# Optimization experiments

Hardware: AMD Instinct MI355X
Metric: run time of the kernel (lower is better)

## Reference

```python
import jax, jax.numpy as jnp
import numpy as np

B, H, E, K = 8192, 1024, 8, 2


def setup_inputs() -> dict:
    key = jax.random.key(0)
    k1, k2, k3 = jax.random.split(key, 3)
    x = jax.random.normal(k1, (B, H), dtype=jnp.float32)
    gate_w = jax.random.normal(k2, (H, E), dtype=jnp.float32) / np.sqrt(H)
    expert_w = jax.random.normal(k3, (E, H, H), dtype=jnp.float32) / np.sqrt(H)
    return {"x": x, "gate_w": gate_w, "expert_w": expert_w}


def reference(x, gate_w, expert_w):
    # Gate: logits over experts, top-k routing, softmax over the k selected logits
    logits = x @ gate_w                               # [B, E]
    top_w, top_idx = jax.lax.top_k(logits, K)         # [B, K]
    top_w = jax.nn.softmax(top_w, axis=-1)            # softmax over the K selected
    # Combine weights scattered back to [B, E]; zero for unselected experts
    combine = jnp.zeros((x.shape[0], expert_w.shape[0]), dtype=x.dtype)
    combine = combine.at[jnp.arange(x.shape[0])[:, None], top_idx].add(top_w)
    # Expert GEMMs (dense dispatch reference: every expert on every token,
    # masked/weighted by combine; mathematically identical to gather/scatter)
    expert_out = jnp.einsum('bh,eho->beo', x, expert_w)   # [B, E, H]
    out = jnp.einsum('be,beo->bo', combine, expert_out)   # [B, H]
    return out
```

## Files before the change

### kernel.cpp

```cpp
#include <hip/hip_runtime.h>
#include <hip/hip_bf16.h>
#include <stdint.h>

#define B_TOK 8192
#define H_DIM 1024
#define E_NUM 8
#define NSLOT (2 * B_TOK)

typedef __attribute__((ext_vector_type(8))) short short8;
typedef __attribute__((ext_vector_type(4))) float floatx4;

__device__ __forceinline__ unsigned short f32_to_bf16_rne(float f) {
  union { float f; uint32_t u; } v; v.f = f;
  uint32_t u = v.u;
  uint32_t r = u + 0x7FFFu + ((u >> 16) & 1u);
  return (unsigned short)(r >> 16);
}
__device__ __forceinline__ float bf16_to_f32(unsigned short s) {
  union { uint32_t u; float f; } v; v.u = ((uint32_t)s) << 16;
  return v.f;
}

__global__ __launch_bounds__(256) void prep_kernel(const float* __restrict__ x,
                                                   const float* __restrict__ gw,
                                                   const float* __restrict__ ew,
                                                   unsigned short* __restrict__ xb,
                                                   unsigned short* __restrict__ wt,
                                                   int2* __restrict__ re,
                                                   float2* __restrict__ rw) {
  __shared__ float smem[E_NUM * 1028];
  int bid = blockIdx.x;
  int tid = threadIdx.x;
  if (bid < 2048) {
    float (*tile)[65] = (float(*)[65])smem;
    int e = bid >> 8;
    int n0 = ((bid >> 4) & 15) * 64, k0 = (bid & 15) * 64;
    const float* wb = ew + ((size_t)e * H_DIM + k0) * H_DIM + n0;
    unsigned short* wtb = wt + ((size_t)e * H_DIM + n0) * H_DIM + k0;
    int rr = tid >> 4, c4 = tid & 15;
#pragma unroll
    for (int j = 0; j < 4; ++j) {
      int r = rr + j * 16;
      float4 v = *(const float4*)(wb + (size_t)r * H_DIM + c4 * 4);
      tile[c4 * 4 + 0][r] = v.x;
      tile[c4 * 4 + 1][r] = v.y;
      tile[c4 * 4 + 2][r] = v.z;
      tile[c4 * 4 + 3][r] = v.w;
    }
    __syncthreads();
#pragma unroll
    for (int j = 0; j < 4; ++j) {
      int nr = rr + j * 16;
      float4 v = *(const float4*)&tile[nr][c4 * 4];
      ushort4 o;
      o.x = f32_to_bf16_rne(v.x); o.y = f32_to_bf16_rne(v.y);
      o.z = f32_to_bf16_rne(v.z); o.w = f32_to_bf16_rne(v.w);
      *(ushort4*)(wtb + (size_t)nr * H_DIM + c4 * 4) = o;
    }
  } else {
    int rb = bid - 2048;
    float (*gws)[1028] = (float(*)[1028])smem;
#pragma unroll
    for (int it = 0; it < 8; ++it) {
      int i4 = it * 256 + tid;
      float4 v = ((const float4*)gw)[i4];
      int h = i4 >> 1, e0 = (i4 & 1) * 4;
      gws[e0 + 0][h] = v.x;
      gws[e0 + 1][h] = v.y;
      gws[e0 + 2][h] = v.z;
      gws[e0 + 3][h] = v.w;
    }
    __syncthreads();
    int wid = tid >> 6, lane = tid & 63;
    for (int t = 0; t < 4; ++t) {
      int b = rb * 16 + wid * 4 + t;
      const float4* xr = (const float4*)(x + (size_t)b * H_DIM);
      ushort4* xbr = (ushort4*)(xb + (size_t)b * H_DIM);
      float acc[E_NUM];
#pragma unroll
      for (int e = 0; e < E_NUM; e++) acc[e] = 0.f;
#pragma unroll
      for (int it = 0; it < 4; ++it) {
        int c4 = it * 64 + lane;
        float4 v = xr[c4];
        ushort4 o;
        o.x = f32_to_bf16_rne(v.x); o.y = f32_to_bf16_rne(v.y);
        o.z = f32_to_bf16_rne(v.z); o.w = f32_to_bf16_rne(v.w);
        xbr[c4] = o;
        int h = c4 * 4;
#pragma unroll
        for (int e = 0; e < E_NUM; e++) {
          float4 g = *(const float4*)&gws[e][h];
          acc[e] += v.x * g.x + v.y * g.y + v.z * g.z + v.w * g.w;
        }
      }
#pragma unroll
      for (int e = 0; e < E_NUM; e++) {
#pragma unroll
        for (int off = 32; off; off >>= 1) acc[e] += __shfl_xor(acc[e], off, 64);
      }
      if (lane == 0) {
        int e0 = 0; float v0 = acc[0];
#pragma unroll
        for (int e = 1; e < E_NUM; e++) if (acc[e] > v0) { v0 = acc[e]; e0 = e; }
        int e1 = -1; float v1 = -1e30f;
#pragma unroll
        for (int e = 0; e < E_NUM; e++) if (e != e0 && acc[e] > v1) { v1 = acc[e]; e1 = e; }
        float s = expf(v1 - v0);
        float w0 = 1.0f / (1.0f + s);
        re[b] = make_int2(e0, e1);
        rw[b] = make_float2(w0, s * w0);
      }
    }
  }
}

__global__ __launch_bounds__(1024) void compact_kernel(const int2* __restrict__ re,
                                                       int* __restrict__ slot_tok,
                                                       int* __restrict__ yslot,
                                                       int* __restrict__ ebase,
                                                       int* __restrict__ ecnt) {
  __shared__ int wcnt[8][16];
  __shared__ int bless[16];
  int e = blockIdx.x;
  int tid = threadIdx.x, wid = tid >> 6, lane = tid & 63;
  int cless = 0;
  int flag[8];
  unsigned long long mm[8];
#pragma unroll
  for (int it = 0; it < 8; ++it) {
    int2 ee = re[it * 1024 + tid];
    cless += (ee.x < e) + (ee.y < e);
    bool f0 = (ee.x == e), f1 = (ee.y == e);
    flag[it] = f0 ? 1 : (f1 ? 2 : 0);
    mm[it] = __ballot(f0 || f1);
    if (lane == 0) wcnt[it][wid] = __popcll(mm[it]);
  }
#pragma unroll
  for (int off = 32; off; off >>= 1) cless += __shfl_xor(cless, off, 64);
  if (lane == 0) bless[wid] = cless;
  __syncthreads();
  int base = 0;
#pragma unroll
  for (int i = 0; i < 16; ++i) base += bless[i];
  int run = 0;
#pragma unroll
  for (int it = 0; it < 8; ++it) {
    int wbase = 0, total = 0;
#pragma unroll
    for (int i = 0; i < 16; ++i) { int v = wcnt[it][i]; if (i < wid) wbase += v; total += v; }
    if (flag[it]) {
      int pre = __popcll(mm[it] & ((1ull << lane) - 1ull));
      int s = base + run + wbase + pre;
      int t = it * 1024 + tid;
      slot_tok[s] = t;
      yslot[2 * t + (flag[it] == 1 ? 0 : 1)] = s;
    }
    run += total;
  }
  if (tid == 0) { ebase[e] = base; ecnt[e] = run; }
}

__device__ __forceinline__ void async_ld16(const void* g, void* l) {
  __builtin_amdgcn_global_load_lds((const __attribute__((address_space(1))) void*)g,
                                   (__attribute__((address_space(3))) void*)l, 16, 0, 0);
}

__global__ __launch_bounds__(256, 3) void moe_gemm_kernel(
    const unsigned short* __restrict__ xb,
    const unsigned short* __restrict__ wt,
    const int* __restrict__ ebase,
    const int* __restrict__ ecnt,
    const int* __restrict__ slot_tok,
    unsigned short* __restrict__ y) {
  int e = blockIdx.z;
  int c = ecnt[e];
  int m_idx = ((blockIdx.y >> 3) << 3) + blockIdx.x;
  int n_idx = blockIdx.y & 7;
  int m0 = m_idx * 128;
  if (m0 >= c) return;
  int base = ebase[e];
  int n0 = n_idx * 128;

  __shared__ __align__(16) unsigned short As[128 * 64];
  __shared__ __align__(16) unsigned short Bs[128 * 64];

  int tid = threadIdx.x, wid = tid >> 6, lane = tid & 63;
  int rloc = lane >> 3;
  int cl = lane & 7;
  const int* st = slot_tok + base;

  const unsigned short* gA[4];
  const unsigned short* gB[4];
  unsigned short* lA[4];
  unsigned short* lB[4];
#pragma unroll
  for (int j = 0; j < 4; ++j) {
    int rl = wid * 32 + j * 8 + rloc;
    int g = (cl ^ (rl & 7)) * 8;
    int ra = min(m0 + rl, c - 1);
    gA[j] = xb + (size_t)st[ra] * H_DIM + g;
    gB[j] = wt + ((size_t)e * H_DIM + n0 + rl) * H_DIM + g;
    lA[j] = As + (wid * 32 + j * 8) * 64;
    lB[j] = Bs + (wid * 32 + j * 8) * 64;
  }

  floatx4 acc[4][4];
#pragma unroll
  for (int a = 0; a < 4; ++a)
#pragma unroll
    for (int b = 0; b < 4; ++b)
#pragma unroll
      for (int q = 0; q < 4; ++q) acc[a][b][q] = 0.0f;

  int wm = (wid >> 1) * 64, wn = (wid & 1) * 64;
  int mr = lane & 15, kg = lane >> 4;
  int sw = mr & 7;

  for (int ks = 0; ks < 16; ++ks) {
    __syncthreads();
#pragma unroll
    for (int j = 0; j < 4; ++j) {
      async_ld16(gA[j], lA[j]);
      async_ld16(gB[j], lB[j]);
    }
#pragma unroll
    for (int j = 0; j < 4; ++j) { gA[j] += 64; gB[j] += 64; }
    __syncthreads();
#pragma unroll
    for (int kk = 0; kk < 2; ++kk) {
      int cb = ((kk * 4 + kg) ^ sw) * 8;
      short8 af[4], bfr[4];
#pragma unroll
      for (int t = 0; t < 4; ++t) {
        af[t]  = *(const short8*)(const void*)(As + (wm + t * 16 + mr) * 64 + cb);
        bfr[t] = *(const short8*)(const void*)(Bs + (wn + t * 16 + mr) * 64 + cb);
      }
#pragma unroll
      for (int tm = 0; tm < 4; ++tm)
#pragma unroll
        for (int tn = 0; tn < 4; ++tn)
          acc[tm][tn] = __builtin_amdgcn_mfma_f32_16x16x32_bf16(af[tm], bfr[tn], acc[tm][tn], 0, 0, 0);
    }
  }

#pragma unroll
  for (int tm = 0; tm < 4; ++tm) {
#pragma unroll
    for (int q = 0; q < 4; ++q) {
      int r = m0 + wm + tm * 16 + kg * 4 + q;
      if (r < c) {
        unsigned short* yrow = y + (size_t)(base + r) * H_DIM + n0 + wn + mr;
#pragma unroll
        for (int tn = 0; tn < 4; ++tn) yrow[tn * 16] = f32_to_bf16_rne(acc[tm][tn][q]);
      }
    }
  }
}

__global__ __launch_bounds__(256) void combine_kernel(const unsigned short* __restrict__ y,
                                                      const int* __restrict__ yslot,
                                                      const float2* __restrict__ rw,
                                                      float* __restrict__ out) {
  int wid = threadIdx.x >> 6, lane = threadIdx.x & 63;
  int t = blockIdx.x * 4 + wid;
  int s0 = yslot[2 * t], s1 = yslot[2 * t + 1];
  float2 w = rw[t];
  const ushort4* y0 = (const ushort4*)(y + (size_t)s0 * H_DIM);
  const ushort4* y1 = (const ushort4*)(y + (size_t)s1 * H_DIM);
  float4* o = (float4*)(out + (size_t)t * H_DIM);
  ushort4 a[4], b[4];
#pragma unroll
  for (int j = 0; j < 4; ++j) {
    int i = j * 64 + lane;
    a[j] = y0[i];
    b[j] = y1[i];
  }
#pragma unroll
  for (int j = 0; j < 4; ++j) {
    int i = j * 64 + lane;
    float4 r;
    r.x = w.x * bf16_to_f32(a[j].x) + w.y * bf16_to_f32(b[j].x);
    r.y = w.x * bf16_to_f32(a[j].y) + w.y * bf16_to_f32(b[j].y);
    r.z = w.x * bf16_to_f32(a[j].z) + w.y * bf16_to_f32(b[j].z);
    r.w = w.x * bf16_to_f32(a[j].w) + w.y * bf16_to_f32(b[j].w);
    o[i] = r;
  }
}

extern "C" void kernel_launch(void* const* d_in, const int* in_sizes, int n_in,
                              void* d_out, int out_size, void* d_ws, size_t ws_size,
                              hipStream_t stream) {
  const float* x  = (const float*)d_in[0];
  const float* gw = (const float*)d_in[1];
  const float* ew = (const float*)d_in[2];
  float* out = (float*)d_out;

  char* ws = (char*)d_ws;
  unsigned short* xb = (unsigned short*)ws;
  unsigned short* wt = (unsigned short*)(ws + (size_t)16 * 1024 * 1024);
  unsigned short* y  = (unsigned short*)(ws + (size_t)32 * 1024 * 1024);
  char* p = ws + (size_t)64 * 1024 * 1024;
  int2*   re       = (int2*)p;
  float2* rw       = (float2*)(p + (64 << 10));
  int*    slot_tok = (int*)(p + (128 << 10));
  int*    yslot    = (int*)(p + (192 << 10));
  int*    ebase    = (int*)(p + (256 << 10));
  int*    ecnt     = (int*)(p + (256 << 10) + 64);

  prep_kernel<<<2560, 256, 0, stream>>>(x, gw, ew, xb, wt, re, rw);
  compact_kernel<<<E_NUM, 1024, 0, stream>>>(re, slot_tok, yslot, ebase, ecnt);
  moe_gemm_kernel<<<dim3(8, 64, E_NUM), 256, 0, stream>>>(
      xb, wt, ebase, ecnt, slot_tok, y);
  combine_kernel<<<B_TOK / 4, 256, 0, stream>>>(y, yslot, rw, out);
}
```

Measured before the change: 170.5 us.

## Widen MoE GEMM tile to 128x256 and batch gate rows in prep

```diff
diff --git a/kernel.cpp b/kernel.cpp
--- a/kernel.cpp
+++ b/kernel.cpp
@@ -72,40 +72,51 @@
     }
     __syncthreads();
     int wid = tid >> 6, lane = tid & 63;
-    for (int t = 0; t < 4; ++t) {
-      int b = rb * 16 + wid * 4 + t;
-      const float4* xr = (const float4*)(x + (size_t)b * H_DIM);
-      ushort4* xbr = (ushort4*)(xb + (size_t)b * H_DIM);
-      float acc[E_NUM];
-#pragma unroll
-      for (int e = 0; e < E_NUM; e++) acc[e] = 0.f;
-#pragma unroll
-      for (int it = 0; it < 4; ++it) {
-        int c4 = it * 64 + lane;
-        float4 v = xr[c4];
+    int b0 = rb * 16 + wid * 4;
+    const float4* xr0 = (const float4*)(x + (size_t)(b0 + 0) * H_DIM);
+    const float4* xr1 = (const float4*)(x + (size_t)(b0 + 1) * H_DIM);
+    const float4* xr2 = (const float4*)(x + (size_t)(b0 + 2) * H_DIM);
+    const float4* xr3 = (const float4*)(x + (size_t)(b0 + 3) * H_DIM);
+    const float4* xr[4] = {xr0, xr1, xr2, xr3};
+    float acc[4][E_NUM];
+#pragma unroll
+    for (int t = 0; t < 4; ++t)
+#pragma unroll
+      for (int e = 0; e < E_NUM; e++) acc[t][e] = 0.f;
+#pragma unroll
+    for (int it = 0; it < 4; ++it) {
+      int c4 = it * 64 + lane;
+      int h = c4 * 4;
+      float4 g[E_NUM];
+#pragma unroll
+      for (int e = 0; e < E_NUM; e++) g[e] = *(const float4*)&gws[e][h];
+#pragma unroll
+      for (int t = 0; t < 4; ++t) {
+        float4 v = xr[t][c4];
         ushort4 o;
         o.x = f32_to_bf16_rne(v.x); o.y = f32_to_bf16_rne(v.y);
         o.z = f32_to_bf16_rne(v.z); o.w = f32_to_bf16_rne(v.w);
-        xbr[c4] = o;
-        int h = c4 * 4;
-#pragma unroll
-        for (int e = 0; e < E_NUM; e++) {
-          float4 g = *(const float4*)&gws[e][h];
-          acc[e] += v.x * g.x + v.y * g.y + v.z * g.z + v.w * g.w;
-        }
+        ((ushort4*)(xb + (size_t)(b0 + t) * H_DIM))[c4] = o;
+#pragma unroll
+        for (int e = 0; e < E_NUM; e++)
+          acc[t][e] += v.x * g[e].x + v.y * g[e].y + v.z * g[e].z + v.w * g[e].w;
       }
+    }
+#pragma unroll
+    for (int t = 0; t < 4; ++t) {
 #pragma unroll
       for (int e = 0; e < E_NUM; e++) {
 #pragma unroll
-        for (int off = 32; off; off >>= 1) acc[e] += __shfl_xor(acc[e], off, 64);
+        for (int off = 32; off; off >>= 1) acc[t][e] += __shfl_xor(acc[t][e], off, 64);
       }
       if (lane == 0) {
-        int e0 = 0; float v0 = acc[0];
-#pragma unroll
-        for (int e = 1; e < E_NUM; e++) if (acc[e] > v0) { v0 = acc[e]; e0 = e; }
+        int b = b0 + t;
+        int e0 = 0; float v0 = acc[t][0];
+#pragma unroll
+        for (int e = 1; e < E_NUM; e++) if (acc[t][e] > v0) { v0 = acc[t][e]; e0 = e; }
         int e1 = -1; float v1 = -1e30f;
 #pragma unroll
-        for (int e = 0; e < E_NUM; e++) if (e != e0 && acc[e] > v1) { v1 = acc[e]; e1 = e; }
+        for (int e = 0; e < E_NUM; e++) if (e != e0 && acc[t][e] > v1) { v1 = acc[t][e]; e1 = e; }
         float s = expf(v1 - v0);
         float w0 = 1.0f / (1.0f + s);
         re[b] = make_int2(e0, e1);
@@ -166,7 +177,7 @@
                                    (__attribute__((address_space(3))) void*)l, 16, 0, 0);
 }
 
-__global__ __launch_bounds__(256, 3) void moe_gemm_kernel(
+__global__ __launch_bounds__(256, 2) void moe_gemm_kernel(
     const unsigned short* __restrict__ xb,
     const unsigned short* __restrict__ wt,
     const int* __restrict__ ebase,
@@ -175,15 +186,13 @@
     unsigned short* __restrict__ y) {
   int e = blockIdx.z;
   int c = ecnt[e];
-  int m_idx = ((blockIdx.y >> 3) << 3) + blockIdx.x;
-  int n_idx = blockIdx.y & 7;
-  int m0 = m_idx * 128;
+  int m0 = blockIdx.y * 128;
   if (m0 >= c) return;
   int base = ebase[e];
-  int n0 = n_idx * 128;
+  int n0 = blockIdx.x * 256;
 
   __shared__ __align__(16) unsigned short As[128 * 64];
-  __shared__ __align__(16) unsigned short Bs[128 * 64];
+  __shared__ __align__(16) unsigned short Bs[256 * 64];
 
   int tid = threadIdx.x, wid = tid >> 6, lane = tid & 63;
   int rloc = lane >> 3;
@@ -191,55 +200,62 @@
   const int* st = slot_tok + base;
 
   const unsigned short* gA[4];
-  const unsigned short* gB[4];
+  const unsigned short* gB[8];
   unsigned short* lA[4];
-  unsigned short* lB[4];
+  unsigned short* lB[8];
 #pragma unroll
   for (int j = 0; j < 4; ++j) {
     int rl = wid * 32 + j * 8 + rloc;
     int g = (cl ^ (rl & 7)) * 8;
     int ra = min(m0 + rl, c - 1);
     gA[j] = xb + (size_t)st[ra] * H_DIM + g;
+    lA[j] = As + (wid * 32 + j * 8) * 64;
+  }
+#pragma unroll
+  for (int j = 0; j < 8; ++j) {
+    int rl = wid * 64 + j * 8 + rloc;
+    int g = (cl ^ (rl & 7)) * 8;
     gB[j] = wt + ((size_t)e * H_DIM + n0 + rl) * H_DIM + g;
-    lA[j] = As + (wid * 32 + j * 8) * 64;
-    lB[j] = Bs + (wid * 32 + j * 8) * 64;
-  }
-
-  floatx4 acc[4][4];
+    lB[j] = Bs + (wid * 64 + j * 8) * 64;
+  }
+
+  floatx4 acc[4][8];
 #pragma unroll
   for (int a = 0; a < 4; ++a)
 #pragma unroll
-    for (int b = 0; b < 4; ++b)
+    for (int b = 0; b < 8; ++b)
 #pragma unroll
       for (int q = 0; q < 4; ++q) acc[a][b][q] = 0.0f;
 
-  int wm = (wid >> 1) * 64, wn = (wid & 1) * 64;
+  int wm = (wid >> 1) * 64, wn = (wid & 1) * 128;
   int mr = lane & 15, kg = lane >> 4;
   int sw = mr & 7;
 
   for (int ks = 0; ks < 16; ++ks) {
     __syncthreads();
 #pragma unroll
-    for (int j = 0; j < 4; ++j) {
-      async_ld16(gA[j], lA[j]);
-      async_ld16(gB[j], lB[j]);
-    }
-#pragma unroll
-    for (int j = 0; j < 4; ++j) { gA[j] += 64; gB[j] += 64; }
+    for (int j = 0; j < 4; ++j) async_ld16(gA[j], lA[j]);
+#pragma unroll
+    for (int j = 0; j < 8; ++j) async_ld16(gB[j], lB[j]);
+#pragma unroll
+    for (int j = 0; j < 4; ++j) gA[j] += 64;
+#pragma unroll
+    for (int j = 0; j < 8; ++j) gB[j] += 64;
     __syncthreads();
 #pragma unroll
     for (int kk = 0; kk < 2; ++kk) {
       int cb = ((kk * 4 + kg) ^ sw) * 8;
-      short8 af[4], bfr[4];
-#pragma unroll
-      for (int t = 0; t < 4; ++t) {
-        af[t]  = *(const short8*)(const void*)(As + (wm + t * 16 + mr) * 64 + cb);
-        bfr[t] = *(const short8*)(const void*)(Bs + (wn + t * 16 + mr) * 64 + cb);
-      }
+      short8 af[4], bfr[8];
+#pragma unroll
+      for (int t = 0; t < 4; ++t)
+        af[t] = *(const short8*)(const void*)(As + (wm + t * 16 + mr) * 64 + cb);
+#pragma unroll
+      for (int u = 0; u < 8; ++u)
+        bfr[u] = *(const short8*)(const void*)(Bs + (wn + u * 16 + mr) * 64 + cb);
 #pragma unroll
       for (int tm = 0; tm < 4; ++tm)
 #pragma unroll
-        for (int tn = 0; tn < 4; ++tn)
+        for (int tn = 0; tn < 8; ++tn)
           acc[tm][tn] = __builtin_amdgcn_mfma_f32_16x16x32_bf16(af[tm], bfr[tn], acc[tm][tn], 0, 0, 0);
     }
   }
@@ -252,7 +268,7 @@
       if (r < c) {
         unsigned short* yrow = y + (size_t)(base + r) * H_DIM + n0 + wn + mr;
 #pragma unroll
-        for (int tn = 0; tn < 4; ++tn) yrow[tn * 16] = f32_to_bf16_rne(acc[tm][tn][q]);
+        for (int tn = 0; tn < 8; ++tn) yrow[tn * 16] = f32_to_bf16_rne(acc[tm][tn][q]);
       }
     }
   }
@@ -310,7 +326,7 @@
 
   prep_kernel<<<2560, 256, 0, stream>>>(x, gw, ew, xb, wt, re, rw);
   compact_kernel<<<E_NUM, 1024, 0, stream>>>(re, slot_tok, yslot, ebase, ecnt);
-  moe_gemm_kernel<<<dim3(8, 64, E_NUM), 256, 0, stream>>>(
+  moe_gemm_kernel<<<dim3(4, 32, E_NUM), 256, 0, stream>>>(
       xb, wt, ebase, ecnt, slot_tok, y);
   combine_kernel<<<B_TOK / 4, 256, 0, stream>>>(y, yslot, rw, out);
 }
```

Measured after the change: 182.1 us. 1.07x slower.

## Fuse combine into GEMM epilogue via weighted atomic adds to zeroed output

Applied to the files above, without the earlier changes.

```diff
diff --git a/kernel.cpp b/kernel.cpp
--- a/kernel.cpp
+++ b/kernel.cpp
@@ -15,10 +15,6 @@
   uint32_t u = v.u;
   uint32_t r = u + 0x7FFFu + ((u >> 16) & 1u);
   return (unsigned short)(r >> 16);
-}
-__device__ __forceinline__ float bf16_to_f32(unsigned short s) {
-  union { uint32_t u; float f; } v; v.u = ((uint32_t)s) << 16;
-  return v.f;
 }
 
 __global__ __launch_bounds__(256) void prep_kernel(const float* __restrict__ x,
@@ -27,7 +23,8 @@
                                                    unsigned short* __restrict__ xb,
                                                    unsigned short* __restrict__ wt,
                                                    int2* __restrict__ re,
-                                                   float2* __restrict__ rw) {
+                                                   float2* __restrict__ rw,
+                                                   float* __restrict__ out) {
   __shared__ float smem[E_NUM * 1028];
   int bid = blockIdx.x;
   int tid = threadIdx.x;
@@ -57,7 +54,7 @@
       o.z = f32_to_bf16_rne(v.z); o.w = f32_to_bf16_rne(v.w);
       *(ushort4*)(wtb + (size_t)nr * H_DIM + c4 * 4) = o;
     }
-  } else {
+  } else if (bid < 2560) {
     int rb = bid - 2048;
     float (*gws)[1028] = (float(*)[1028])smem;
 #pragma unroll
@@ -72,52 +69,70 @@
     }
     __syncthreads();
     int wid = tid >> 6, lane = tid & 63;
-    for (int t = 0; t < 4; ++t) {
-      int b = rb * 16 + wid * 4 + t;
-      const float4* xr = (const float4*)(x + (size_t)b * H_DIM);
-      ushort4* xbr = (ushort4*)(xb + (size_t)b * H_DIM);
-      float acc[E_NUM];
-#pragma unroll
-      for (int e = 0; e < E_NUM; e++) acc[e] = 0.f;
-#pragma unroll
-      for (int it = 0; it < 4; ++it) {
-        int c4 = it * 64 + lane;
-        float4 v = xr[c4];
+    int b0 = rb * 16 + wid * 4;
+    const float4* xr0 = (const float4*)(x + (size_t)(b0 + 0) * H_DIM);
+    const float4* xr1 = (const float4*)(x + (size_t)(b0 + 1) * H_DIM);
+    const float4* xr2 = (const float4*)(x + (size_t)(b0 + 2) * H_DIM);
+    const float4* xr3 = (const float4*)(x + (size_t)(b0 + 3) * H_DIM);
+    const float4* xr[4] = {xr0, xr1, xr2, xr3};
+    float acc[4][E_NUM];
+#pragma unroll
+    for (int t = 0; t < 4; ++t)
+#pragma unroll
+      for (int e = 0; e < E_NUM; e++) acc[t][e] = 0.f;
+#pragma unroll
+    for (int it = 0; it < 4; ++it) {
+      int c4 = it * 64 + lane;
+      int h = c4 * 4;
+      float4 g[E_NUM];
+#pragma unroll
+      for (int e = 0; e < E_NUM; e++) g[e] = *(const float4*)&gws[e][h];
+#pragma unroll
+      for (int t = 0; t < 4; ++t) {
+        float4 v = xr[t][c4];
         ushort4 o;
         o.x = f32_to_bf16_rne(v.x); o.y = f32_to_bf16_rne(v.y);
         o.z = f32_to_bf16_rne(v.z); o.w = f32_to_bf16_rne(v.w);
-        xbr[c4] = o;
-        int h = c4 * 4;
-#pragma unroll
-        for (int e = 0; e < E_NUM; e++) {
-          float4 g = *(const float4*)&gws[e][h];
-          acc[e] += v.x * g.x + v.y * g.y + v.z * g.z + v.w * g.w;
-        }
-      }
+        ((ushort4*)(xb + (size_t)(b0 + t) * H_DIM))[c4] = o;
+#pragma unroll
+        for (int e = 0; e < E_NUM; e++)
+          acc[t][e] += v.x * g[e].x + v.y * g[e].y + v.z * g[e].z + v.w * g[e].w;
+      }
+    }
+#pragma unroll
+    for (int t = 0; t < 4; ++t) {
 #pragma unroll
       for (int e = 0; e < E_NUM; e++) {
 #pragma unroll
-        for (int off = 32; off; off >>= 1) acc[e] += __shfl_xor(acc[e], off, 64);
+        for (int off = 32; off; off >>= 1) acc[t][e] += __shfl_xor(acc[t][e], off, 64);
       }
       if (lane == 0) {
-        int e0 = 0; float v0 = acc[0];
-#pragma unroll
-        for (int e = 1; e < E_NUM; e++) if (acc[e] > v0) { v0 = acc[e]; e0 = e; }
+        int b = b0 + t;
+        int e0 = 0; float v0 = acc[t][0];
+#pragma unroll
+        for (int e = 1; e < E_NUM; e++) if (acc[t][e] > v0) { v0 = acc[t][e]; e0 = e; }
         int e1 = -1; float v1 = -1e30f;
 #pragma unroll
-        for (int e = 0; e < E_NUM; e++) if (e != e0 && acc[e] > v1) { v1 = acc[e]; e1 = e; }
+        for (int e = 0; e < E_NUM; e++) if (e != e0 && acc[t][e] > v1) { v1 = acc[t][e]; e1 = e; }
         float s = expf(v1 - v0);
         float w0 = 1.0f / (1.0f + s);
         re[b] = make_int2(e0, e1);
         rw[b] = make_float2(w0, s * w0);
       }
     }
+  } else {
+    int zb = bid - 2560;
+    float4* o = (float4*)(out + (size_t)zb * 16384);
+    float4 z = make_float4(0.f, 0.f, 0.f, 0.f);
+#pragma unroll
+    for (int j = 0; j < 16; ++j) o[j * 256 + tid] = z;
   }
 }
 
 __global__ __launch_bounds__(1024) void compact_kernel(const int2* __restrict__ re,
+                                                       const float2* __restrict__ rw,
                                                        int* __restrict__ slot_tok,
-                                                       int* __restrict__ yslot,
+                                                       float* __restrict__ slot_w,
                                                        int* __restrict__ ebase,
                                                        int* __restrict__ ecnt) {
   __shared__ int wcnt[8][16];
@@ -154,7 +169,8 @@
       int s = base + run + wbase + pre;
       int t = it * 1024 + tid;
       slot_tok[s] = t;
-      yslot[2 * t + (flag[it] == 1 ? 0 : 1)] = s;
+      float2 w = rw[t];
+      slot_w[s] = (flag[it] == 1) ? w.x : w.y;
     }
     run += total;
   }
@@ -172,7 +188,8 @@
     const int* __restrict__ ebase,
     const int* __restrict__ ecnt,
     const int* __restrict__ slot_tok,
-    unsigned short* __restrict__ y) {
+    const float* __restrict__ slot_w,
+    float* __restrict__ out) {
   int e = blockIdx.z;
   int c = ecnt[e];
   int m_idx = ((blockIdx.y >> 3) << 3) + blockIdx.x;
@@ -189,6 +206,7 @@
   int rloc = lane >> 3;
   int cl = lane & 7;
   const int* st = slot_tok + base;
+  const float* sw_ = slot_w + base;
 
   const unsigned short* gA[4];
   const unsigned short* gB[4];
@@ -250,41 +268,13 @@
     for (int q = 0; q < 4; ++q) {
       int r = m0 + wm + tm * 16 + kg * 4 + q;
       if (r < c) {
-        unsigned short* yrow = y + (size_t)(base + r) * H_DIM + n0 + wn + mr;
-#pragma unroll
-        for (int tn = 0; tn < 4; ++tn) yrow[tn * 16] = f32_to_bf16_rne(acc[tm][tn][q]);
-      }
-    }
-  }
-}
-
-__global__ __launch_bounds__(256) void combine_kernel(const unsigned short* __restrict__ y,
-                                                      const int* __restrict__ yslot,
-                                                      const float2* __restrict__ rw,
-                                                      float* __restrict__ out) {
-  int wid = threadIdx.x >> 6, lane = threadIdx.x & 63;
-  int t = blockIdx.x * 4 + wid;
-  int s0 = yslot[2 * t], s1 = yslot[2 * t + 1];
-  float2 w = rw[t];
-  const ushort4* y0 = (const ushort4*)(y + (size_t)s0 * H_DIM);
-  const ushort4* y1 = (const ushort4*)(y + (size_t)s1 * H_DIM);
-  float4* o = (float4*)(out + (size_t)t * H_DIM);
-  ushort4 a[4], b[4];
-#pragma unroll
-  for (int j = 0; j < 4; ++j) {
-    int i = j * 64 + lane;
-    a[j] = y0[i];
-    b[j] = y1[i];
-  }
-#pragma unroll
-  for (int j = 0; j < 4; ++j) {
-    int i = j * 64 + lane;
-    float4 r;
-    r.x = w.x * bf16_to_f32(a[j].x) + w.y * bf16_to_f32(b[j].x);
-    r.y = w.x * bf16_to_f32(a[j].y) + w.y * bf16_to_f32(b[j].y);
-    r.z = w.x * bf16_to_f32(a[j].z) + w.y * bf16_to_f32(b[j].z);
-    r.w = w.x * bf16_to_f32(a[j].w) + w.y * bf16_to_f32(b[j].w);
-    o[i] = r;
+        int tok = st[r];
+        float w = sw_[r];
+        float* orow = out + (size_t)tok * H_DIM + n0 + wn + mr;
+#pragma unroll
+        for (int tn = 0; tn < 4; ++tn) atomicAdd(orow + tn * 16, w * acc[tm][tn][q]);
+      }
+    }
   }
 }
 
@@ -299,18 +289,16 @@
   char* ws = (char*)d_ws;
   unsigned short* xb = (unsigned short*)ws;
   unsigned short* wt = (unsigned short*)(ws + (size_t)16 * 1024 * 1024);
-  unsigned short* y  = (unsigned short*)(ws + (size_t)32 * 1024 * 1024);
-  char* p = ws + (size_t)64 * 1024 * 1024;
+  char* p = ws + (size_t)32 * 1024 * 1024;
   int2*   re       = (int2*)p;
   float2* rw       = (float2*)(p + (64 << 10));
   int*    slot_tok = (int*)(p + (128 << 10));
-  int*    yslot    = (int*)(p + (192 << 10));
+  float*  slot_w   = (float*)(p + (192 << 10));
   int*    ebase    = (int*)(p + (256 << 10));
   int*    ecnt     = (int*)(p + (256 << 10) + 64);
 
-  prep_kernel<<<2560, 256, 0, stream>>>(x, gw, ew, xb, wt, re, rw);
-  compact_kernel<<<E_NUM, 1024, 0, stream>>>(re, slot_tok, yslot, ebase, ecnt);
+  prep_kernel<<<3072, 256, 0, stream>>>(x, gw, ew, xb, wt, re, rw, out);
+  compact_kernel<<<E_NUM, 1024, 0, stream>>>(re, rw, slot_tok, slot_w, ebase, ecnt);
   moe_gemm_kernel<<<dim3(8, 64, E_NUM), 256, 0, stream>>>(
-      xb, wt, ebase, ecnt, slot_tok, y);
-  combine_kernel<<<B_TOK / 4, 256, 0, stream>>>(y, yslot, rw, out);
-}
+      xb, wt, ebase, ecnt, slot_tok, slot_w, out);
+}
```

After: 203.1 us. 1.19x slower.
